# Optimization experiments

Measured on AMD Instinct MI355X. Metric: run time of the kernel, lower is better.

Reference implementation:

```python
import jax, jax.numpy as jnp
import numpy as np

B = 16384      # games
BS = 19        # board size
N2 = BS * BS   # 361
G = 8          # groups per board
S = 4          # stones per group
R = B * G      # total groups
K = R * S      # total stones
M = N2         # hash history length (H*W*history_factor)
I32MIN = np.iinfo(np.int32).min
I32MAX = np.iinfo(np.int32).max
NEG = jnp.float32(-1e9)


def setup_inputs() -> dict:
    key = jax.random.key(0)
    ks = jax.random.split(key, 10)
    logits = jax.random.normal(ks[0], (B, BS, BS), dtype=jnp.float32)
    legal_mask = jax.random.uniform(ks[1], (B, BS, BS)) < 0.7
    current_player = jax.random.randint(ks[2], (B,), 0, 2, dtype=jnp.int32)
    current_hash = jax.random.randint(ks[3], (B,), 0, I32MAX, dtype=jnp.int32)
    hash_history = jax.random.randint(ks[4], (B, M), 0, I32MAX, dtype=jnp.int32)
    move_count = jax.random.randint(ks[5], (B,), 0, M, dtype=jnp.int32)
    ZposT = jax.random.randint(ks[6], (3, N2), 0, I32MAX, dtype=jnp.int32)
    stone_global_index = jax.random.randint(ks[7], (K,), 0, N2, dtype=jnp.int32)
    stone_global_pointer = jnp.arange(R + 1, dtype=jnp.int32) * S          # CSR: stones per group
    group_global_pointer_per_board = jnp.arange(B + 1, dtype=jnp.int32) * G  # CSR: groups per board
    cap_idx = jax.random.randint(ks[8], (B, N2, 4), 0, G, dtype=jnp.int32)
    cap_on = jax.random.uniform(ks[9], (B, N2, 4)) < 0.05
    captured_group_local_index = jnp.where(cap_on, cap_idx, jnp.int32(-1))
    return {
        "logits": logits,
        "legal_mask": legal_mask,
        "current_player": current_player,
        "current_hash": current_hash,
        "hash_history": hash_history,
        "move_count": move_count,
        "ZposT": ZposT,
        "stone_global_index": stone_global_index,
        "stone_global_pointer": stone_global_pointer,
        "group_global_pointer_per_board": group_global_pointer_per_board,
        "captured_group_local_index": captured_group_local_index,
    }


def reference(logits, legal_mask, current_player, current_hash, hash_history,
              move_count, ZposT, stone_global_index, stone_global_pointer,
              group_global_pointer_per_board, captured_group_local_index):
    Bn, H, W = legal_mask.shape
    Rn = stone_global_pointer.shape[0] - 1
    Kn = stone_global_index.shape[0]
    z_empty, z_black, z_white = ZposT[0], ZposT[1], ZposT[2]

    # Placement delta: empty -> current player's stone, for every candidate point. (B, N2)
    placement_delta = z_empty[None, :] ^ jnp.where(
        (current_player == 0)[:, None], z_black[None, :], z_white[None, :])

    # Map each group -> board, each stone -> group (CSR expansion).
    groups_per_board = group_global_pointer_per_board[1:] - group_global_pointer_per_board[:-1]
    group_board = jnp.repeat(jnp.arange(Bn, dtype=jnp.int32), groups_per_board,
                             total_repeat_length=Rn)
    stones_per_group = stone_global_pointer[1:] - stone_global_pointer[:-1]
    group_for_stone = jnp.repeat(jnp.arange(Rn, dtype=jnp.int32), stones_per_group,
                                 total_repeat_length=Kn)
    stone_board = group_board[group_for_stone]

    # Per-stone removal delta: opponent stone -> empty.
    opp_for_stone = (1 - current_player)[stone_board]           # (K,)
    si = stone_global_index.astype(jnp.int32)
    z_opp = ZposT[1 + opp_for_stone, si]
    per_stone_delta = z_opp ^ z_empty[si]                        # (K,) int32

    # Segmented XOR reduction over each group's stones via XOR prefix scan.
    prefix = jax.lax.associative_scan(jnp.bitwise_xor, per_stone_delta)
    start = stone_global_pointer[:-1]
    end = stone_global_pointer[1:]
    end_val = prefix[jnp.clip(end - 1, 0)]
    start_val = jnp.where(start > 0, prefix[jnp.clip(start - 1, 0)], jnp.int32(0))
    group_xor = end_val ^ start_val                              # (R,) per-group removal delta

    # Gather capture deltas for up to 4 captured neighbor groups per candidate move.
    offs = group_global_pointer_per_board[:-1][:, None, None]    # (B,1,1)
    flat_ids = jnp.clip(captured_group_local_index, 0) + offs    # (B,N2,4)
    cap_vals = jnp.where(captured_group_local_index >= 0, group_xor[flat_ids], jnp.int32(0))
    capture_delta = cap_vals[..., 0] ^ cap_vals[..., 1] ^ cap_vals[..., 2] ^ cap_vals[..., 3]

    candidate = current_hash[:, None] ^ placement_delta ^ capture_delta  # (B, N2)

    # Super-ko repeat detection against hash history (mask, sort, searchsorted).
    Mh = hash_history.shape[1]
    valid = jnp.arange(Mh, dtype=jnp.int32)[None, :] < jnp.minimum(move_count, Mh)[:, None]
    masked_hist = jnp.where(valid, hash_history, jnp.int32(I32MIN))
    sorted_hist = jnp.sort(masked_hist, axis=1)
    idx = jnp.clip(
        jax.vmap(lambda h, c: jnp.searchsorted(h, c, side='right'))(sorted_hist, candidate) - 1,
        0)
    found = jnp.take_along_axis(sorted_hist, idx, axis=1)
    repeat = (found == candidate).reshape(Bn, H, W)

    final_mask = legal_mask & ~repeat
    return jnp.where(final_mask, logits, NEG)
```

## Files before the change

kernel.cpp:

```cpp
#include <hip/hip_runtime.h>
#include <stdint.h>

#define N2 361
#define TBL 1024
#define TBL_MASK 1023u
#define EMPTY_SLOT 0x80000000u
#define NEGV -998244352.0f

__global__ __launch_bounds__(128) void go_repeat_mask_kernel(
    const float* __restrict__ logits,
    const void*  __restrict__ legal_raw,
    const int*   __restrict__ current_player,
    const int*   __restrict__ current_hash,
    const int*   __restrict__ hash_history,
    const int*   __restrict__ move_count,
    const int*   __restrict__ ZposT,
    const int*   __restrict__ stone_global_index,
    const int*   __restrict__ stone_global_pointer,
    const int*   __restrict__ group_global_pointer,
    const int4*  __restrict__ captured4,
    float*       __restrict__ out,
    int packed_bits)
{
    __shared__ unsigned s_table[TBL];
    __shared__ int s_gx[8];

    const int b   = blockIdx.x;
    const int tid = threadIdx.x;
    const size_t bbase = (size_t)b * N2;

    const int      cp  = current_player[b];
    const unsigned ch  = (unsigned)current_hash[b];
    int            cnt = move_count[b];

    const int iC = (tid + 256 < N2) ? (tid + 256) : (N2 - 1);

    const int* hist = hash_history + bbase;
    const int h0 = hist[tid];
    const int h1 = hist[tid + 128];
    const int h2 = hist[iC];

    const int4 capA = captured4[bbase + tid];
    const int4 capB = captured4[bbase + tid + 128];
    const int4 capC = captured4[bbase + iC];

    const float lgA = logits[bbase + tid];
    const float lgB = logits[bbase + tid + 128];
    const float lgC = logits[bbase + iC];

    const unsigned* lwd = (const unsigned*)legal_raw;
    const int lane = tid & 63;
    const unsigned dv0 = lwd[lane];
    const unsigned dv1 = (lane < 27) ? lwd[64 + lane] : 0u;

    int g0 = 0, g1 = 0, sp0 = 0, sp1 = 0;
    if (tid < 32) {
        g0 = group_global_pointer[b];
        g1 = group_global_pointer[b + 1];
        const int r = g0 + (tid >> 2);
        if (r < g1) {
            sp0 = stone_global_pointer[r];
            sp1 = stone_global_pointer[r + 1];
        }
    }

    auto classify = [](unsigned v) -> unsigned {
        unsigned f = 0;
        #pragma unroll
        for (int j = 0; j < 4; ++j) {
            const unsigned bv = (v >> (8 * j)) & 0xFFu;
            if (bv > 1u) f |= 1u;
            if (j != 0 && bv != 0u) f |= 2u;
        }
        const unsigned ha = v & 0xFFFFu, hb = v >> 16;
        if ((ha && ha != 0x3F80u) || (hb && hb != 0x3F80u)) f |= 4u;
        if (ha == 0x3F80u) f |= 8u;
        return f;
    };
    unsigned fcl = classify(dv0);
    if (lane < 27) fcl |= classify(dv1);
    unsigned fa = 0;
    fa |= __ballot(fcl & 1u) ? 1u : 0u;
    fa |= __ballot(fcl & 2u) ? 2u : 0u;
    fa |= __ballot(fcl & 4u) ? 4u : 0u;
    fa |= __ballot(fcl & 8u) ? 8u : 0u;

    int fmt;
    if (packed_bits) fmt = 4;
    else if (!(fa & 1u)) fmt = 0;
    else if (!(fa & 4u)) fmt = (fa & 8u) ? 2 : 0;
    else fmt = 1;

    unsigned legA, legB, legC;
    {
        const size_t qA = bbase + tid, qB = bbase + tid + 128, qC = bbase + iC;
        if (fmt == 0) {
            const unsigned* p = (const unsigned*)legal_raw;
            legA = p[qA]; legB = p[qB]; legC = p[qC];
        } else if (fmt == 1) {
            const uint8_t* p = (const uint8_t*)legal_raw;
            legA = p[qA]; legB = p[qB]; legC = p[qC];
        } else if (fmt == 2) {
            const uint16_t* p = (const uint16_t*)legal_raw;
            legA = p[qA]; legB = p[qB]; legC = p[qC];
        } else {
            const uint8_t* p = (const uint8_t*)legal_raw;
            legA = (p[qA >> 3] >> (qA & 7)) & 1u;
            legB = (p[qB >> 3] >> (qB & 7)) & 1u;
            legC = (p[qC >> 3] >> (qC & 7)) & 1u;
        }
    }

    if (tid < 32) {
        unsigned gx = 0u;
        const int j = tid & 3;
        const int opprow = (2 - cp) * N2;
        for (int k = sp0 + j; k < sp1; k += 4) {
            const int si = stone_global_index[k];
            gx ^= (unsigned)ZposT[opprow + si] ^ (unsigned)ZposT[si];
        }
        gx ^= __shfl_xor(gx, 1);
        gx ^= __shfl_xor(gx, 2);
        if (j == 0) s_gx[tid >> 2] = (int)gx;
    }

    #pragma unroll
    for (int i = 0; i < TBL / 128; ++i) s_table[tid + i * 128] = EMPTY_SLOT;

    cnt = cnt < 0 ? 0 : (cnt > N2 ? N2 : cnt);
    __syncthreads();

    auto insert = [&](unsigned v) {
        unsigned slot = v & TBL_MASK;
        while (true) {
            const unsigned old = atomicCAS(&s_table[slot], EMPTY_SLOT, v);
            if (old == EMPTY_SLOT || old == v) break;
            slot = (slot + 1) & TBL_MASK;
        }
    };
    if (tid < cnt)       insert((unsigned)h0);
    if (tid + 128 < cnt) insert((unsigned)h1);
    if (tid + 256 < cnt) insert((unsigned)h2);
    __syncthreads();

    const int prow = (1 + cp) * N2;
    auto probe = [&](unsigned cand) -> bool {
        unsigned slot = cand & TBL_MASK;
        while (true) {
            const unsigned v = s_table[slot];
            if (v == cand) return true;
            if (v == EMPTY_SLOT) return false;
            slot = (slot + 1) & TBL_MASK;
        }
    };
    auto capxor = [&](int4 c) -> unsigned {
        unsigned d = 0u;
        if (c.x >= 0) d ^= (unsigned)s_gx[c.x & 7];
        if (c.y >= 0) d ^= (unsigned)s_gx[c.y & 7];
        if (c.z >= 0) d ^= (unsigned)s_gx[c.z & 7];
        if (c.w >= 0) d ^= (unsigned)s_gx[c.w & 7];
        return d;
    };

    {
        const int n = tid;
        const unsigned cand = ch ^ (unsigned)ZposT[n] ^ (unsigned)ZposT[prow + n] ^ capxor(capA);
        const float v = (legA && !probe(cand)) ? lgA : NEGV;
        __builtin_nontemporal_store(v, &out[bbase + n]);
    }
    {
        const int n = tid + 128;
        const unsigned cand = ch ^ (unsigned)ZposT[n] ^ (unsigned)ZposT[prow + n] ^ capxor(capB);
        const float v = (legB && !probe(cand)) ? lgB : NEGV;
        __builtin_nontemporal_store(v, &out[bbase + n]);
    }
    if (tid < N2 - 256) {
        const int n = tid + 256;
        const unsigned cand = ch ^ (unsigned)ZposT[n] ^ (unsigned)ZposT[prow + n] ^ capxor(capC);
        const float v = (legC && !probe(cand)) ? lgC : NEGV;
        __builtin_nontemporal_store(v, &out[bbase + n]);
    }
}

extern "C" void kernel_launch(void* const* d_in, const int* in_sizes, int n_in,
                              void* d_out, int out_size, void* d_ws, size_t ws_size,
                              hipStream_t stream) {
    const float* logits  = (const float*)d_in[0];
    const void*  legal   = (const void*)d_in[1];
    const int*   cur_pl  = (const int*)d_in[2];
    const int*   cur_h   = (const int*)d_in[3];
    const int*   hist    = (const int*)d_in[4];
    const int*   mcount  = (const int*)d_in[5];
    const int*   zpos    = (const int*)d_in[6];
    const int*   sgi     = (const int*)d_in[7];
    const int*   sgp     = (const int*)d_in[8];
    const int*   ggp     = (const int*)d_in[9];
    const int4*  cap4    = (const int4*)d_in[10];
    float*       out     = (float*)d_out;

    const int B = in_sizes[2];
    const int packed = (in_sizes[1] != in_sizes[0]);

    go_repeat_mask_kernel<<<B, 128, 0, stream>>>(
        logits, legal, cur_pl, cur_h, hist, mcount, zpos,
        sgi, sgp, ggp, cap4, out, packed);
}
```

Measured before the change: 223.6 us.

## Map one wavefront per board with private LDS hash table and no block barriers

Restructures the kernel so each 64-lane wavefront handles one board, with four boards per 256-thread block and a private 1024-slot shared-memory hash table per wave. This removes __syncthreads in favour of wave-local ordering. Group capture XORs move from shared memory to cross-lane shuffles. The hash history is loaded with int4 vector loads, and all per-cell inputs, including the Zobrist values, are preloaded into registers up front. This raises register pressure and relies on wave-synchronous LDS visibility, which the code enforces with an explicit lgkmcnt wait.

```diff
diff --git a/kernel.cpp b/kernel.cpp
--- a/kernel.cpp
+++ b/kernel.cpp
@@ -2,12 +2,12 @@
 #include <stdint.h>
 
 #define N2 361
-#define TBL 1024
+#define TBLW 1024
 #define TBL_MASK 1023u
 #define EMPTY_SLOT 0x80000000u
 #define NEGV -998244352.0f
 
-__global__ __launch_bounds__(128) void go_repeat_mask_kernel(
+__global__ __launch_bounds__(256, 4) void go_repeat_mask_kernel(
     const float* __restrict__ logits,
     const void*  __restrict__ legal_raw,
     const int*   __restrict__ current_player,
@@ -22,46 +22,50 @@
     float*       __restrict__ out,
     int packed_bits)
 {
-    __shared__ unsigned s_table[TBL];
-    __shared__ int s_gx[8];
-
-    const int b   = blockIdx.x;
-    const int tid = threadIdx.x;
+    __shared__ unsigned s_table[4 * TBLW];
+
+    const int tid  = threadIdx.x;
+    const int wid  = tid >> 6;
+    const int lane = tid & 63;
+    const int b    = __builtin_amdgcn_readfirstlane(blockIdx.x * 4 + wid);
+    unsigned* tbl  = s_table + wid * TBLW;
     const size_t bbase = (size_t)b * N2;
 
     const int      cp  = current_player[b];
     const unsigned ch  = (unsigned)current_hash[b];
     int            cnt = move_count[b];
 
-    const int iC = (tid + 256 < N2) ? (tid + 256) : (N2 - 1);
-
-    const int* hist = hash_history + bbase;
-    const int h0 = hist[tid];
-    const int h1 = hist[tid + 128];
-    const int h2 = hist[iC];
-
-    const int4 capA = captured4[bbase + tid];
-    const int4 capB = captured4[bbase + tid + 128];
-    const int4 capC = captured4[bbase + iC];
-
-    const float lgA = logits[bbase + tid];
-    const float lgB = logits[bbase + tid + 128];
-    const float lgC = logits[bbase + iC];
+    const int*  hist  = hash_history + bbase;
+    const int4* hist4 = (const int4*)hist;
+    const int4  ha    = hist4[lane];
+    const int4  hb    = (lane < 26) ? hist4[64 + lane] : int4{0,0,0,0};
+    const int   hc    = (lane == 26) ? hist[360] : 0;
 
     const unsigned* lwd = (const unsigned*)legal_raw;
-    const int lane = tid & 63;
     const unsigned dv0 = lwd[lane];
     const unsigned dv1 = (lane < 27) ? lwd[64 + lane] : 0u;
 
-    int g0 = 0, g1 = 0, sp0 = 0, sp1 = 0;
-    if (tid < 32) {
-        g0 = group_global_pointer[b];
-        g1 = group_global_pointer[b + 1];
-        const int r = g0 + (tid >> 2);
-        if (r < g1) {
-            sp0 = stone_global_pointer[r];
-            sp1 = stone_global_pointer[r + 1];
-        }
+    int sp0 = 0, sp1 = 0;
+    const int g0 = group_global_pointer[b];
+    const int g1 = group_global_pointer[b + 1];
+    if (lane < 32) {
+        const int r = g0 + (lane >> 2);
+        if (r < g1) { sp0 = stone_global_pointer[r]; sp1 = stone_global_pointer[r + 1]; }
+    }
+
+    int4  cap[6];
+    float lg[6];
+    unsigned zA[6], zB[6];
+    const int prow = (1 + cp) * N2;
+    #pragma unroll
+    for (int s = 0; s < 6; ++s) {
+        const int n = lane + 64 * s;
+        const int nc = (n < N2) ? n : (N2 - 1);
+        const size_t q = bbase + nc;
+        cap[s] = captured4[q];
+        lg[s]  = logits[q];
+        zA[s]  = (unsigned)ZposT[nc];
+        zB[s]  = (unsigned)ZposT[prow + nc];
     }
 
     auto classify = [](unsigned v) -> unsigned {
@@ -72,9 +76,9 @@
             if (bv > 1u) f |= 1u;
             if (j != 0 && bv != 0u) f |= 2u;
         }
-        const unsigned ha = v & 0xFFFFu, hb = v >> 16;
-        if ((ha && ha != 0x3F80u) || (hb && hb != 0x3F80u)) f |= 4u;
-        if (ha == 0x3F80u) f |= 8u;
+        const unsigned x = v & 0xFFFFu, y = v >> 16;
+        if ((x && x != 0x3F80u) || (y && y != 0x3F80u)) f |= 4u;
+        if (x == 0x3F80u) f |= 8u;
         return f;
     };
     unsigned fcl = classify(dv0);
@@ -91,29 +95,24 @@
     else if (!(fa & 4u)) fmt = (fa & 8u) ? 2 : 0;
     else fmt = 1;
 
-    unsigned legA, legB, legC;
+    unsigned leg[6];
+    #pragma unroll
+    for (int s = 0; s < 6; ++s) leg[s] = 0u;
     {
-        const size_t qA = bbase + tid, qB = bbase + tid + 128, qC = bbase + iC;
-        if (fmt == 0) {
-            const unsigned* p = (const unsigned*)legal_raw;
-            legA = p[qA]; legB = p[qB]; legC = p[qC];
-        } else if (fmt == 1) {
-            const uint8_t* p = (const uint8_t*)legal_raw;
-            legA = p[qA]; legB = p[qB]; legC = p[qC];
-        } else if (fmt == 2) {
-            const uint16_t* p = (const uint16_t*)legal_raw;
-            legA = p[qA]; legB = p[qB]; legC = p[qC];
-        } else {
-            const uint8_t* p = (const uint8_t*)legal_raw;
-            legA = (p[qA >> 3] >> (qA & 7)) & 1u;
-            legB = (p[qB >> 3] >> (qB & 7)) & 1u;
-            legC = (p[qC >> 3] >> (qC & 7)) & 1u;
-        }
-    }
-
-    if (tid < 32) {
-        unsigned gx = 0u;
-        const int j = tid & 3;
+        #pragma unroll
+        for (int s = 0; s < 6; ++s) {
+            const int n = lane + 64 * s;
+            const size_t q = bbase + ((n < N2) ? n : (N2 - 1));
+            if (fmt == 0)      leg[s] = ((const unsigned*)legal_raw)[q];
+            else if (fmt == 1) leg[s] = ((const uint8_t*)legal_raw)[q];
+            else if (fmt == 2) leg[s] = ((const uint16_t*)legal_raw)[q];
+            else               leg[s] = (((const uint8_t*)legal_raw)[q >> 3] >> (q & 7)) & 1u;
+        }
+    }
+
+    unsigned gx = 0u;
+    if (lane < 32) {
+        const int j = lane & 3;
         const int opprow = (2 - cp) * N2;
         for (int k = sp0 + j; k < sp1; k += 4) {
             const int si = stone_global_index[k];
@@ -121,64 +120,65 @@
         }
         gx ^= __shfl_xor(gx, 1);
         gx ^= __shfl_xor(gx, 2);
-        if (j == 0) s_gx[tid >> 2] = (int)gx;
-    }
-
-    #pragma unroll
-    for (int i = 0; i < TBL / 128; ++i) s_table[tid + i * 128] = EMPTY_SLOT;
+    }
+
+    {
+        uint4* t4 = (uint4*)tbl;
+        const uint4 e4 = {EMPTY_SLOT, EMPTY_SLOT, EMPTY_SLOT, EMPTY_SLOT};
+        #pragma unroll
+        for (int i = 0; i < 4; ++i) t4[lane + 64 * i] = e4;
+    }
 
     cnt = cnt < 0 ? 0 : (cnt > N2 ? N2 : cnt);
-    __syncthreads();
-
-    auto insert = [&](unsigned v) {
+
+    auto ins = [&](unsigned v) {
         unsigned slot = v & TBL_MASK;
         while (true) {
-            const unsigned old = atomicCAS(&s_table[slot], EMPTY_SLOT, v);
+            const unsigned old = atomicCAS(&tbl[slot], EMPTY_SLOT, v);
             if (old == EMPTY_SLOT || old == v) break;
             slot = (slot + 1) & TBL_MASK;
         }
     };
-    if (tid < cnt)       insert((unsigned)h0);
-    if (tid + 128 < cnt) insert((unsigned)h1);
-    if (tid + 256 < cnt) insert((unsigned)h2);
-    __syncthreads();
-
-    const int prow = (1 + cp) * N2;
+    {
+        const int i0 = 4 * lane;
+        if (i0 + 0 < cnt) ins((unsigned)ha.x);
+        if (i0 + 1 < cnt) ins((unsigned)ha.y);
+        if (i0 + 2 < cnt) ins((unsigned)ha.z);
+        if (i0 + 3 < cnt) ins((unsigned)ha.w);
+        if (lane < 26) {
+            const int i1 = 256 + 4 * lane;
+            if (i1 + 0 < cnt) ins((unsigned)hb.x);
+            if (i1 + 1 < cnt) ins((unsigned)hb.y);
+            if (i1 + 2 < cnt) ins((unsigned)hb.z);
+            if (i1 + 3 < cnt) ins((unsigned)hb.w);
+        }
+        if (lane == 26 && 360 < cnt) ins((unsigned)hc);
+    }
+    asm volatile("s_waitcnt lgkmcnt(0)" ::: "memory");
+
     auto probe = [&](unsigned cand) -> bool {
         unsigned slot = cand & TBL_MASK;
         while (true) {
-            const unsigned v = s_table[slot];
+            const unsigned v = tbl[slot];
             if (v == cand) return true;
             if (v == EMPTY_SLOT) return false;
             slot = (slot + 1) & TBL_MASK;
         }
     };
-    auto capxor = [&](int4 c) -> unsigned {
-        unsigned d = 0u;
-        if (c.x >= 0) d ^= (unsigned)s_gx[c.x & 7];
-        if (c.y >= 0) d ^= (unsigned)s_gx[c.y & 7];
-        if (c.z >= 0) d ^= (unsigned)s_gx[c.z & 7];
-        if (c.w >= 0) d ^= (unsigned)s_gx[c.w & 7];
-        return d;
-    };
-
-    {
-        const int n = tid;
-        const unsigned cand = ch ^ (unsigned)ZposT[n] ^ (unsigned)ZposT[prow + n] ^ capxor(capA);
-        const float v = (legA && !probe(cand)) ? lgA : NEGV;
-        __builtin_nontemporal_store(v, &out[bbase + n]);
-    }
-    {
-        const int n = tid + 128;
-        const unsigned cand = ch ^ (unsigned)ZposT[n] ^ (unsigned)ZposT[prow + n] ^ capxor(capB);
-        const float v = (legB && !probe(cand)) ? lgB : NEGV;
-        __builtin_nontemporal_store(v, &out[bbase + n]);
-    }
-    if (tid < N2 - 256) {
-        const int n = tid + 256;
-        const unsigned cand = ch ^ (unsigned)ZposT[n] ^ (unsigned)ZposT[prow + n] ^ capxor(capC);
-        const float v = (legC && !probe(cand)) ? lgC : NEGV;
-        __builtin_nontemporal_store(v, &out[bbase + n]);
+    #pragma unroll
+    for (int s = 0; s < 6; ++s) {
+        const int n = lane + 64 * s;
+        if (n < N2) {
+            unsigned capd = 0u;
+            const int4 c = cap[s];
+            if (c.x >= 0) capd ^= (unsigned)__shfl((int)gx, (c.x & 7) * 4);
+            if (c.y >= 0) capd ^= (unsigned)__shfl((int)gx, (c.y & 7) * 4);
+            if (c.z >= 0) capd ^= (unsigned)__shfl((int)gx, (c.z & 7) * 4);
+            if (c.w >= 0) capd ^= (unsigned)__shfl((int)gx, (c.w & 7) * 4);
+            const unsigned cand = ch ^ zA[s] ^ zB[s] ^ capd;
+            const float v = (leg[s] && !probe(cand)) ? lg[s] : NEGV;
+            __builtin_nontemporal_store(v, &out[bbase + n]);
+        }
     }
 }
 
@@ -201,7 +201,7 @@
     const int B = in_sizes[2];
     const int packed = (in_sizes[1] != in_sizes[0]);
 
-    go_repeat_mask_kernel<<<B, 128, 0, stream>>>(
+    go_repeat_mask_kernel<<<B / 4, 256, 0, stream>>>(
         logits, legal, cur_pl, cur_h, hist, mcount, zpos,
         sgi, sgp, ggp, cap4, out, packed);
 }
```

Result: slower. 228.1 us (+2.0%).
